# Kernel tuning notes

Hardware: AMD Instinct MI355X
Metric: run time of the kernel (lower is better)

The kernel has to match this reference:

```python
import jax, jax.numpy as jnp
import numpy as np

B, H, T, D = 2, 16, 2048, 64
BASE_WINDOW = 256
FULL = 999999


def _make_window_sizes(num_heads=H, base_window=BASE_WINDOW):
    ws = []
    for h in range(num_heads):
        if h < num_heads // 4:
            ws.append(base_window)
        elif h < num_heads // 2:
            ws.append(base_window * 2)
        elif h < 3 * num_heads // 4:
            ws.append(base_window * 4)
        else:
            ws.append(FULL)
    return jnp.asarray(ws, dtype=jnp.int32)


def setup_inputs() -> dict:
    key = jax.random.key(0)
    kq, kk, kv = jax.random.split(key, 3)
    Q = jax.random.normal(kq, (B, H, T, D), dtype=jnp.float32)
    K = jax.random.normal(kk, (B, H, T, D), dtype=jnp.float32)
    V = jax.random.normal(kv, (B, H, T, D), dtype=jnp.float32)
    return {"Q": Q, "K": K, "V": V, "window_sizes": _make_window_sizes()}


def reference(Q, K, V, window_sizes):
    b, h, t, d = Q.shape
    scale = 1.0 / np.sqrt(d).astype(np.float32)
    idx = jnp.arange(t, dtype=jnp.int32)
    diff = idx[:, None] - idx[None, :]  # [T, T], q_idx - kv_idx
    # causal & |q-k| <= w  ==  0 <= diff <= w  (per head)
    mask = (diff >= 0) & (diff[None, :, :] <= window_sizes[:, None, None])  # [H, T, T]
    scores = jnp.einsum('bhqd,bhkd->bhqk', Q, K) * scale  # [B, H, T, T]
    scores = jnp.where(mask[None], scores, -jnp.inf)
    attn = jax.nn.softmax(scores, axis=-1)
    return jnp.einsum('bhqk,bhkd->bhqd', attn, V)
```

## Files before the change

kernel.cpp:

```cpp
#include <hip/hip_runtime.h>
#include <hip/hip_bf16.h>


constexpr int Bc = 2, Hc = 16, Tc = 2048, Dc = 64;
constexpr int BQ = 64;
constexpr int BK = 32;
constexpr float QSCALE = 0.125f * 1.44269504088896340736f;
constexpr float CMAX = 16.0f;

constexpr size_t KB_OFF = 256;
constexpr size_t VB_OFF = 256 + (size_t)Bc * Hc * Tc * Dc * 2;
constexpr int HEADE = Tc * Dc;

constexpr int KOFF = 0;
constexpr int VOFF = 8192;

typedef __attribute__((ext_vector_type(8))) short short8;
typedef __attribute__((ext_vector_type(4))) float float4v;
typedef __attribute__((ext_vector_type(2))) unsigned int uint2v;

#if defined(__has_builtin)
#if __has_builtin(__builtin_amdgcn_exp2f)
#define EXP2 __builtin_amdgcn_exp2f
#endif
#endif
#ifndef EXP2
#define EXP2 exp2f
#endif

__device__ inline unsigned f2bf_u(float f) {
    union { float f; unsigned u; } v; v.f = f;
    return (v.u + 0x7fffu + ((v.u >> 16) & 1u)) >> 16;
}

__device__ inline short8 pack8(const float* t) {
    short8 r;
#pragma unroll
    for (int j = 0; j < 8; j++) r[j] = (short)f2bf_u(t[j]);
    return r;
}

__device__ inline unsigned pk_bf16(float a, float b) {
    __hip_bfloat162 h = __float22bfloat162_rn(make_float2(a, b));
    union { __hip_bfloat162 h; unsigned u; } v; v.h = h;
    return v.u;
}

__device__ inline short8 mk8(unsigned a0, unsigned a1, unsigned a2, unsigned a3) {
    union { unsigned u[4]; short8 s; } v;
    v.u[0] = a0; v.u[1] = a1; v.u[2] = a2; v.u[3] = a3;
    return v.s;
}

__global__ __launch_bounds__(256)
void preconv_kernel(const float* __restrict__ K, const float* __restrict__ V,
                    unsigned short* __restrict__ Kb, unsigned short* __restrict__ Vtb) {
    const int blk = blockIdx.x;
    const int tid = threadIdx.x;
    if (blk < 2048) {
        const int base = blk * 2048 + tid * 8;
        float4v a = *(const float4v*)(K + base);
        float4v b = *(const float4v*)(K + base + 4);
        float t[8] = {a[0], a[1], a[2], a[3], b[0], b[1], b[2], b[3]};
        *(short8*)(Kb + base) = pack8(t);
    } else {
        __shared__ float tile[64][65];
        const int blk2 = blk - 2048;
        const int bh = blk2 >> 5;
        const int t0 = (blk2 & 31) * 64;
        const float* src = V + (size_t)bh * HEADE + (size_t)t0 * Dc;
#pragma unroll
        for (int i = 0; i < 4; i++) {
            const int r = (tid >> 4) + i * 16;
            const int d4 = (tid & 15) * 4;
            float4v v4 = *(const float4v*)(src + r * Dc + d4);
            tile[r][d4] = v4[0]; tile[r][d4 + 1] = v4[1];
            tile[r][d4 + 2] = v4[2]; tile[r][d4 + 3] = v4[3];
        }
        __syncthreads();
        unsigned short* dst = Vtb + (size_t)bh * HEADE + t0;
#pragma unroll
        for (int i = 0; i < 2; i++) {
            const int d = (tid >> 3) + 32 * i;
            const int c = tid & 7;
            float t[8];
#pragma unroll
            for (int j = 0; j < 8; j++) t[j] = tile[c * 8 + j][d];
            *(short8*)(dst + (size_t)d * Tc + c * 8) = pack8(t);
        }
    }
}

__global__ __launch_bounds__(256, 4)
void dswa_kernel(const float* __restrict__ Q,
                 const unsigned short* __restrict__ Kb,
                 const unsigned short* __restrict__ Vtb,
                 const int* __restrict__ wsz,
                 float* __restrict__ O) {
    __shared__ __align__(16) unsigned short LDS[18432];

    const int tid  = threadIdx.x;
    const int wave = tid >> 6;
    const int g    = wave >> 1;
    const int wq   = wave & 1;
    const int lane = tid & 63;
    const int quad = lane >> 4;
    const int l16  = lane & 15;

    unsigned short* Kg = &LDS[KOFF + g * 4096];
    unsigned short* Vg = &LDS[VOFF + g * 5120];

    const int l128 = tid & 127;
    const int krow = l128 >> 2;
    const int kcol = (l128 & 3) * 16;
    const int vrow = l128 >> 1;
    const int vcol = (l128 & 1) * 16;

    const int blk  = blockIdx.x;
    const int ci   = blk & 255;
    const int slot = blk >> 8;
    const int b    = ci & 1;
    const int q5   = (ci >> 1) & 31;
    const int hh   = ci >> 6;
    const int h    = (3 - slot) * 4 + hh;
    const int qt   = (slot == 0) ? q5 : 31 - q5;
    const int q0   = qt * BQ;
    const int win  = wsz[h];

    const size_t headoff = (size_t)(b * Hc + h) * HEADE;
    const float* Qp = Q + headoff;
    const unsigned short* Kbh = Kb + headoff;
    const unsigned short* Vbh = Vtb + headoff;
    float* Op = O + headoff;

    short8 qf[2][2];
#pragma unroll
    for (int s = 0; s < 2; s++) {
        const int qrow = q0 + wq * 32 + s * 16 + l16;
#pragma unroll
        for (int c = 0; c < 2; c++) {
            const float* src = Qp + (size_t)qrow * Dc + c * 32 + quad * 8;
            float4v a = *(const float4v*)src;
            float4v d4 = *(const float4v*)(src + 4);
            float t[8] = {a[0]*QSCALE, a[1]*QSCALE, a[2]*QSCALE, a[3]*QSCALE,
                          d4[0]*QSCALE, d4[1]*QSCALE, d4[2]*QSCALE, d4[3]*QSCALE};
            qf[s][c] = pack8(t);
        }
    }

    float4v acc[2][4];
#pragma unroll
    for (int s = 0; s < 2; s++)
#pragma unroll
        for (int nb = 0; nb < 4; nb++) acc[s][nb] = (float4v){0.f, 0.f, 0.f, 0.f};
    float lp0 = 0.0f, lp1 = 0.0f;

    const int kv_lo = (max(0, q0 - win)) & ~(BK - 1);
    const int n_tiles = (q0 + BQ - kv_lo) >> 5;
    const int IT = (n_tiles + 1) >> 1;

    const int kv0g = kv_lo + g * BK;
    const unsigned short* kgp = Kbh + (size_t)(kv0g + krow) * Dc + kcol;
    const unsigned short* vgp = Vbh + (size_t)vrow * Tc + kv0g + vcol;

    short8 kr0, kr1, vr0, vr1;
    if (g < n_tiles) {
        kr0 = *(const short8*)(kgp);
        kr1 = *(const short8*)(kgp + 8);
        vr0 = *(const short8*)(vgp);
        vr1 = *(const short8*)(vgp + 8);
    }
    kgp += 64 * Dc; vgp += 64;

    for (int t = 0; t < IT; ++t) {
        const int ti = g + 2 * t;
        const bool act = ti < n_tiles;
        const int kv0 = kv_lo + ti * BK;
        unsigned short* Kl = Kg + (t & 1) * 2048;
        unsigned short* Vt = Vg + (t & 1) * 2560;

        if (act) {
            const int ks = (krow & 7) << 3;
            *(short8*)&Kl[krow * 64 + (kcol ^ ks)] = kr0;
            *(short8*)&Kl[krow * 64 + ((kcol + 8) ^ ks)] = kr1;
            *(short8*)&Vt[vrow * 40 + vcol] = vr0;
            *(short8*)&Vt[vrow * 40 + vcol + 8] = vr1;
        }
        __syncthreads();

        if (ti + 2 < n_tiles) {
            kr0 = *(const short8*)(kgp);
            kr1 = *(const short8*)(kgp + 8);
            vr0 = *(const short8*)(vgp);
            vr1 = *(const short8*)(vgp + 8);
        }
        kgp += 64 * Dc; vgp += 64;

        if (act) {
            float4v sT0[2], sT1[2];
#pragma unroll
            for (int mb = 0; mb < 2; mb++) {
                float4v c0 = {-CMAX, -CMAX, -CMAX, -CMAX};
                float4v c1 = {-CMAX, -CMAX, -CMAX, -CMAX};
#pragma unroll
                for (int ch = 0; ch < 2; ch++) {
                    const int row = mb * 16 + l16;
                    short8 kf = *(short8*)&Kl[row * 64 +
                                              ((ch * 32 + quad * 8) ^ ((row & 7) << 3))];
                    c0 = __builtin_amdgcn_mfma_f32_16x16x32_bf16(kf, qf[0][ch], c0, 0, 0, 0);
                    c1 = __builtin_amdgcn_mfma_f32_16x16x32_bf16(kf, qf[1][ch], c1, 0, 0, 0);
                }
                sT0[mb] = c0; sT1[mb] = c1;
            }

            short8 pf0, pf1;
            {
                const int rs = q0 + wq * 32;
                const bool interior = (kv0 + 31 <= rs) && (rs + 15 - kv0 <= win);
                if (!interior) {
                    const int dbase = rs + l16 - kv0 - quad * 4;
#pragma unroll
                    for (int mb = 0; mb < 2; mb++)
#pragma unroll
                        for (int r = 0; r < 4; r++) {
                            const unsigned diff = (unsigned)(dbase - mb * 16 - r);
                            sT0[mb][r] = (diff <= (unsigned)win) ? sT0[mb][r] : -3.0e38f;
                        }
                }
                unsigned w[4];
#pragma unroll
                for (int mb = 0; mb < 2; mb++) {
                    float p0 = EXP2(sT0[mb][0]);
                    float p1 = EXP2(sT0[mb][1]);
                    float p2 = EXP2(sT0[mb][2]);
                    float p3 = EXP2(sT0[mb][3]);
                    lp0 += (p0 + p1) + (p2 + p3);
                    w[2 * mb]     = pk_bf16(p0, p1);
                    w[2 * mb + 1] = pk_bf16(p2, p3);
                }
                uint2v pa = __builtin_amdgcn_permlane32_swap(w[0], w[2], false, false);
                uint2v c02 = __builtin_amdgcn_permlane16_swap(pa[0], pa[1], false, false);
                uint2v pb = __builtin_amdgcn_permlane32_swap(w[1], w[3], false, false);
                uint2v c13 = __builtin_amdgcn_permlane16_swap(pb[0], pb[1], false, false);
                pf0 = mk8(c02[0], c13[0], c02[1], c13[1]);
            }
            {
                const int rs = q0 + wq * 32 + 16;
                const bool interior = (kv0 + 31 <= rs) && (rs + 15 - kv0 <= win);
                if (!interior) {
                    const int dbase = rs + l16 - kv0 - quad * 4;
#pragma unroll
                    for (int mb = 0; mb < 2; mb++)
#pragma unroll
                        for (int r = 0; r < 4; r++) {
                            const unsigned diff = (unsigned)(dbase - mb * 16 - r);
                            sT1[mb][r] = (diff <= (unsigned)win) ? sT1[mb][r] : -3.0e38f;
                        }
                }
                unsigned w[4];
#pragma unroll
                for (int mb = 0; mb < 2; mb++) {
                    float p0 = EXP2(sT1[mb][0]);
                    float p1 = EXP2(sT1[mb][1]);
                    float p2 = EXP2(sT1[mb][2]);
                    float p3 = EXP2(sT1[mb][3]);
                    lp1 += (p0 + p1) + (p2 + p3);
                    w[2 * mb]     = pk_bf16(p0, p1);
                    w[2 * mb + 1] = pk_bf16(p2, p3);
                }
                uint2v pa = __builtin_amdgcn_permlane32_swap(w[0], w[2], false, false);
                uint2v c02 = __builtin_amdgcn_permlane16_swap(pa[0], pa[1], false, false);
                uint2v pb = __builtin_amdgcn_permlane32_swap(w[1], w[3], false, false);
                uint2v c13 = __builtin_amdgcn_permlane16_swap(pb[0], pb[1], false, false);
                pf1 = mk8(c02[0], c13[0], c02[1], c13[1]);
            }

#pragma unroll
            for (int nb = 0; nb < 4; nb++) {
                short8 vf = *(short8*)&Vt[(nb * 16 + l16) * 40 + quad * 8];
                acc[0][nb] = __builtin_amdgcn_mfma_f32_16x16x32_bf16(pf0, vf, acc[0][nb], 0, 0, 0);
                acc[1][nb] = __builtin_amdgcn_mfma_f32_16x16x32_bf16(pf1, vf, acc[1][nb], 0, 0, 0);
            }
        }
    }

    lp0 += __shfl_xor(lp0, 16); lp0 += __shfl_xor(lp0, 32);
    lp1 += __shfl_xor(lp1, 16); lp1 += __shfl_xor(lp1, 32);

    __syncthreads();
    float* fl = (float*)LDS;
    if (g == 1) {
#pragma unroll
        for (int s = 0; s < 2; s++) {
            if (quad == 0) fl[(wq * 32 + s * 16 + l16) * 66 + 64] = (s ? lp1 : lp0);
#pragma unroll
            for (int r = 0; r < 4; r++) {
                const int row = wq * 32 + s * 16 + quad * 4 + r;
#pragma unroll
                for (int nb = 0; nb < 4; nb++)
                    fl[row * 66 + nb * 16 + l16] = acc[s][nb][r];
            }
        }
    }
    __syncthreads();
    if (g == 0) {
#pragma unroll
        for (int s = 0; s < 2; s++) {
            const float lps = s ? lp1 : lp0;
#pragma unroll
            for (int r = 0; r < 4; r++) {
                const int row = wq * 32 + s * 16 + quad * 4 + r;
                const float l0 = __shfl(lps, quad * 4 + r);
                const float lt = l0 + fl[row * 66 + 64];
                const float inv = 1.0f / lt;
                float* dst = Op + (size_t)(q0 + row) * Dc;
#pragma unroll
                for (int nb = 0; nb < 4; nb++)
                    dst[nb * 16 + l16] = (acc[s][nb][r] + fl[row * 66 + nb * 16 + l16]) * inv;
            }
        }
    }
}

extern "C" void kernel_launch(void* const* d_in, const int* in_sizes, int n_in,
                              void* d_out, int out_size, void* d_ws, size_t ws_size,
                              hipStream_t stream) {
    (void)in_sizes; (void)n_in; (void)ws_size; (void)out_size;
    const float* Q = (const float*)d_in[0];
    const float* K = (const float*)d_in[1];
    const float* V = (const float*)d_in[2];
    const int* wsz = (const int*)d_in[3];
    float* Out = (float*)d_out;

    unsigned short* Kb  = (unsigned short*)((char*)d_ws + KB_OFF);
    unsigned short* Vtb = (unsigned short*)((char*)d_ws + VB_OFF);

    preconv_kernel<<<dim3(3072), dim3(256), 0, stream>>>(K, V, Kb, Vtb);
    dswa_kernel<<<dim3(1024), dim3(256), 0, stream>>>(Q, Kb, Vtb, wsz, Out);
}
```

Measured before the change: 120.7 us.

## Fuse K bf16 conversion into attention kernel and add MFMA priority hints

Result: no change. 119.3 us (-1.2%).

```diff
diff --git a/kernel.cpp b/kernel.cpp
--- a/kernel.cpp
+++ b/kernel.cpp
@@ -8,8 +8,7 @@
 constexpr float QSCALE = 0.125f * 1.44269504088896340736f;
 constexpr float CMAX = 16.0f;
 
-constexpr size_t KB_OFF = 256;
-constexpr size_t VB_OFF = 256 + (size_t)Bc * Hc * Tc * Dc * 2;
+constexpr size_t VB_OFF = 256;
 constexpr int HEADE = Tc * Dc;
 
 constexpr int KOFF = 0;
@@ -53,47 +52,37 @@
 }
 
 __global__ __launch_bounds__(256)
-void preconv_kernel(const float* __restrict__ K, const float* __restrict__ V,
-                    unsigned short* __restrict__ Kb, unsigned short* __restrict__ Vtb) {
-    const int blk = blockIdx.x;
+void preconv_kernel(const float* __restrict__ V, unsigned short* __restrict__ Vtb) {
+    __shared__ float tile[64][65];
+    const int blk2 = blockIdx.x;
     const int tid = threadIdx.x;
-    if (blk < 2048) {
-        const int base = blk * 2048 + tid * 8;
-        float4v a = *(const float4v*)(K + base);
-        float4v b = *(const float4v*)(K + base + 4);
-        float t[8] = {a[0], a[1], a[2], a[3], b[0], b[1], b[2], b[3]};
-        *(short8*)(Kb + base) = pack8(t);
-    } else {
-        __shared__ float tile[64][65];
-        const int blk2 = blk - 2048;
-        const int bh = blk2 >> 5;
-        const int t0 = (blk2 & 31) * 64;
-        const float* src = V + (size_t)bh * HEADE + (size_t)t0 * Dc;
-#pragma unroll
-        for (int i = 0; i < 4; i++) {
-            const int r = (tid >> 4) + i * 16;
-            const int d4 = (tid & 15) * 4;
-            float4v v4 = *(const float4v*)(src + r * Dc + d4);
-            tile[r][d4] = v4[0]; tile[r][d4 + 1] = v4[1];
-            tile[r][d4 + 2] = v4[2]; tile[r][d4 + 3] = v4[3];
-        }
-        __syncthreads();
-        unsigned short* dst = Vtb + (size_t)bh * HEADE + t0;
-#pragma unroll
-        for (int i = 0; i < 2; i++) {
-            const int d = (tid >> 3) + 32 * i;
-            const int c = tid & 7;
-            float t[8];
-#pragma unroll
-            for (int j = 0; j < 8; j++) t[j] = tile[c * 8 + j][d];
-            *(short8*)(dst + (size_t)d * Tc + c * 8) = pack8(t);
-        }
+    const int bh = blk2 >> 5;
+    const int t0 = (blk2 & 31) * 64;
+    const float* src = V + (size_t)bh * HEADE + (size_t)t0 * Dc;
+#pragma unroll
+    for (int i = 0; i < 4; i++) {
+        const int r = (tid >> 4) + i * 16;
+        const int d4 = (tid & 15) * 4;
+        float4v v4 = *(const float4v*)(src + r * Dc + d4);
+        tile[r][d4] = v4[0]; tile[r][d4 + 1] = v4[1];
+        tile[r][d4 + 2] = v4[2]; tile[r][d4 + 3] = v4[3];
+    }
+    __syncthreads();
+    unsigned short* dst = Vtb + (size_t)bh * HEADE + t0;
+#pragma unroll
+    for (int i = 0; i < 2; i++) {
+        const int d = (tid >> 3) + 32 * i;
+        const int c = tid & 7;
+        float t[8];
+#pragma unroll
+        for (int j = 0; j < 8; j++) t[j] = tile[c * 8 + j][d];
+        *(short8*)(dst + (size_t)d * Tc + c * 8) = pack8(t);
     }
 }
 
 __global__ __launch_bounds__(256, 4)
 void dswa_kernel(const float* __restrict__ Q,
-                 const unsigned short* __restrict__ Kb,
+                 const float* __restrict__ K,
                  const unsigned short* __restrict__ Vtb,
                  const int* __restrict__ wsz,
                  float* __restrict__ O) {
@@ -129,7 +118,7 @@
 
     const size_t headoff = (size_t)(b * Hc + h) * HEADE;
     const float* Qp = Q + headoff;
-    const unsigned short* Kbh = Kb + headoff;
+    const float* Kh = K + headoff;
     const unsigned short* Vbh = Vtb + headoff;
     float* Op = O + headoff;
 
@@ -160,13 +149,16 @@
     const int IT = (n_tiles + 1) >> 1;
 
     const int kv0g = kv_lo + g * BK;
-    const unsigned short* kgp = Kbh + (size_t)(kv0g + krow) * Dc + kcol;
+    const float* kgp = Kh + (size_t)(kv0g + krow) * Dc + kcol;
     const unsigned short* vgp = Vbh + (size_t)vrow * Tc + kv0g + vcol;
 
-    short8 kr0, kr1, vr0, vr1;
+    float4v ka0, ka1, ka2, ka3;
+    short8 vr0, vr1;
     if (g < n_tiles) {
-        kr0 = *(const short8*)(kgp);
-        kr1 = *(const short8*)(kgp + 8);
+        ka0 = *(const float4v*)(kgp);
+        ka1 = *(const float4v*)(kgp + 4);
+        ka2 = *(const float4v*)(kgp + 8);
+        ka3 = *(const float4v*)(kgp + 12);
         vr0 = *(const short8*)(vgp);
         vr1 = *(const short8*)(vgp + 8);
     }
@@ -181,6 +173,10 @@
 
         if (act) {
             const int ks = (krow & 7) << 3;
+            short8 kr0 = mk8(pk_bf16(ka0[0], ka0[1]), pk_bf16(ka0[2], ka0[3]),
+                             pk_bf16(ka1[0], ka1[1]), pk_bf16(ka1[2], ka1[3]));
+            short8 kr1 = mk8(pk_bf16(ka2[0], ka2[1]), pk_bf16(ka2[2], ka2[3]),
+                             pk_bf16(ka3[0], ka3[1]), pk_bf16(ka3[2], ka3[3]));
             *(short8*)&Kl[krow * 64 + (kcol ^ ks)] = kr0;
             *(short8*)&Kl[krow * 64 + ((kcol + 8) ^ ks)] = kr1;
             *(short8*)&Vt[vrow * 40 + vcol] = vr0;
@@ -189,8 +185,10 @@
         __syncthreads();
 
         if (ti + 2 < n_tiles) {
-            kr0 = *(const short8*)(kgp);
-            kr1 = *(const short8*)(kgp + 8);
+            ka0 = *(const float4v*)(kgp);
+            ka1 = *(const float4v*)(kgp + 4);
+            ka2 = *(const float4v*)(kgp + 8);
+            ka3 = *(const float4v*)(kgp + 12);
             vr0 = *(const short8*)(vgp);
             vr1 = *(const short8*)(vgp + 8);
         }
@@ -198,6 +196,7 @@
 
         if (act) {
             float4v sT0[2], sT1[2];
+            __builtin_amdgcn_s_setprio(1);
 #pragma unroll
             for (int mb = 0; mb < 2; mb++) {
                 float4v c0 = {-CMAX, -CMAX, -CMAX, -CMAX};
@@ -212,6 +211,7 @@
                 }
                 sT0[mb] = c0; sT1[mb] = c1;
             }
+            __builtin_amdgcn_s_setprio(0);
 
             short8 pf0, pf1;
             {
@@ -275,12 +275,14 @@
                 pf1 = mk8(c02[0], c13[0], c02[1], c13[1]);
             }
 
+            __builtin_amdgcn_s_setprio(1);
 #pragma unroll
             for (int nb = 0; nb < 4; nb++) {
                 short8 vf = *(short8*)&Vt[(nb * 16 + l16) * 40 + quad * 8];
                 acc[0][nb] = __builtin_amdgcn_mfma_f32_16x16x32_bf16(pf0, vf, acc[0][nb], 0, 0, 0);
                 acc[1][nb] = __builtin_amdgcn_mfma_f32_16x16x32_bf16(pf1, vf, acc[1][nb], 0, 0, 0);
             }
+            __builtin_amdgcn_s_setprio(0);
         }
     }
 
@@ -332,9 +334,8 @@
     const int* wsz = (const int*)d_in[3];
     float* Out = (float*)d_out;
 
-    unsigned short* Kb  = (unsigned short*)((char*)d_ws + KB_OFF);
     unsigned short* Vtb = (unsigned short*)((char*)d_ws + VB_OFF);
 
-    preconv_kernel<<<dim3(3072), dim3(256), 0, stream>>>(K, V, Kb, Vtb);
-    dswa_kernel<<<dim3(1024), dim3(256), 0, stream>>>(Q, Kb, Vtb, wsz, Out);
-}
+    preconv_kernel<<<dim3(1024), dim3(256), 0, stream>>>(V, Vtb);
+    dswa_kernel<<<dim3(1024), dim3(256), 0, stream>>>(Q, K, Vtb, wsz, Out);
+}
```

## Give each wave a private K/V LDS tile and drop per-tile block barriers

Applied to the files above, without the earlier changes.

Result: slower. 140.1 us (+16.1%).

```diff
diff --git a/kernel.cpp b/kernel.cpp
--- a/kernel.cpp
+++ b/kernel.cpp
@@ -11,9 +11,6 @@
 constexpr size_t KB_OFF = 256;
 constexpr size_t VB_OFF = 256 + (size_t)Bc * Hc * Tc * Dc * 2;
 constexpr int HEADE = Tc * Dc;
-
-constexpr int KOFF = 0;
-constexpr int VOFF = 8192;
 
 typedef __attribute__((ext_vector_type(8))) short short8;
 typedef __attribute__((ext_vector_type(4))) float float4v;
@@ -107,14 +104,12 @@
     const int quad = lane >> 4;
     const int l16  = lane & 15;
 
-    unsigned short* Kg = &LDS[KOFF + g * 4096];
-    unsigned short* Vg = &LDS[VOFF + g * 5120];
-
-    const int l128 = tid & 127;
-    const int krow = l128 >> 2;
-    const int kcol = (l128 & 3) * 16;
-    const int vrow = l128 >> 1;
-    const int vcol = (l128 & 1) * 16;
+    unsigned short* Kw = &LDS[wave * 4608];
+    unsigned short* Vw = &LDS[wave * 4608 + 2048];
+
+    const int krow  = lane >> 1;
+    const int kcolh = (lane & 1) * 32;
+    const int vrow  = lane;
 
     const int blk  = blockIdx.x;
     const int ci   = blk & 255;
@@ -156,132 +151,140 @@
     float lp0 = 0.0f, lp1 = 0.0f;
 
     const int kv_lo = (max(0, q0 - win)) & ~(BK - 1);
-    const int n_tiles = (q0 + BQ - kv_lo) >> 5;
-    const int IT = (n_tiles + 1) >> 1;
+    const int C = (q0 + BQ - kv_lo) >> 5;
 
     const int kv0g = kv_lo + g * BK;
-    const unsigned short* kgp = Kbh + (size_t)(kv0g + krow) * Dc + kcol;
-    const unsigned short* vgp = Vbh + (size_t)vrow * Tc + kv0g + vcol;
-
-    short8 kr0, kr1, vr0, vr1;
-    if (g < n_tiles) {
+    const unsigned short* kgp = Kbh + (size_t)(kv0g + krow) * Dc + kcolh;
+    const unsigned short* vgp = Vbh + (size_t)vrow * Tc + kv0g;
+
+    short8 kr0, kr1, kr2, kr3, vr0, vr1, vr2, vr3;
+    if (g < C) {
         kr0 = *(const short8*)(kgp);
         kr1 = *(const short8*)(kgp + 8);
+        kr2 = *(const short8*)(kgp + 16);
+        kr3 = *(const short8*)(kgp + 24);
         vr0 = *(const short8*)(vgp);
         vr1 = *(const short8*)(vgp + 8);
+        vr2 = *(const short8*)(vgp + 16);
+        vr3 = *(const short8*)(vgp + 24);
     }
     kgp += 64 * Dc; vgp += 64;
 
-    for (int t = 0; t < IT; ++t) {
-        const int ti = g + 2 * t;
-        const bool act = ti < n_tiles;
+    for (int ti = g; ti < C; ti += 2) {
         const int kv0 = kv_lo + ti * BK;
-        unsigned short* Kl = Kg + (t & 1) * 2048;
-        unsigned short* Vt = Vg + (t & 1) * 2560;
-
-        if (act) {
+
+        {
             const int ks = (krow & 7) << 3;
-            *(short8*)&Kl[krow * 64 + (kcol ^ ks)] = kr0;
-            *(short8*)&Kl[krow * 64 + ((kcol + 8) ^ ks)] = kr1;
-            *(short8*)&Vt[vrow * 40 + vcol] = vr0;
-            *(short8*)&Vt[vrow * 40 + vcol + 8] = vr1;
-        }
-        __syncthreads();
-
-        if (ti + 2 < n_tiles) {
+            *(short8*)&Kw[krow * 64 + ((kcolh)      ^ ks)] = kr0;
+            *(short8*)&Kw[krow * 64 + ((kcolh + 8)  ^ ks)] = kr1;
+            *(short8*)&Kw[krow * 64 + ((kcolh + 16) ^ ks)] = kr2;
+            *(short8*)&Kw[krow * 64 + ((kcolh + 24) ^ ks)] = kr3;
+            *(short8*)&Vw[vrow * 40 + 0]  = vr0;
+            *(short8*)&Vw[vrow * 40 + 8]  = vr1;
+            *(short8*)&Vw[vrow * 40 + 16] = vr2;
+            *(short8*)&Vw[vrow * 40 + 24] = vr3;
+        }
+
+        if (ti + 2 < C) {
             kr0 = *(const short8*)(kgp);
             kr1 = *(const short8*)(kgp + 8);
+            kr2 = *(const short8*)(kgp + 16);
+            kr3 = *(const short8*)(kgp + 24);
             vr0 = *(const short8*)(vgp);
             vr1 = *(const short8*)(vgp + 8);
+            vr2 = *(const short8*)(vgp + 16);
+            vr3 = *(const short8*)(vgp + 24);
         }
         kgp += 64 * Dc; vgp += 64;
 
-        if (act) {
-            float4v sT0[2], sT1[2];
+        float4v sT0[2], sT1[2];
+        __builtin_amdgcn_s_setprio(1);
+#pragma unroll
+        for (int mb = 0; mb < 2; mb++) {
+            float4v c0 = {-CMAX, -CMAX, -CMAX, -CMAX};
+            float4v c1 = {-CMAX, -CMAX, -CMAX, -CMAX};
+#pragma unroll
+            for (int ch = 0; ch < 2; ch++) {
+                const int row = mb * 16 + l16;
+                short8 kf = *(short8*)&Kw[row * 64 +
+                                          ((ch * 32 + quad * 8) ^ ((row & 7) << 3))];
+                c0 = __builtin_amdgcn_mfma_f32_16x16x32_bf16(kf, qf[0][ch], c0, 0, 0, 0);
+                c1 = __builtin_amdgcn_mfma_f32_16x16x32_bf16(kf, qf[1][ch], c1, 0, 0, 0);
+            }
+            sT0[mb] = c0; sT1[mb] = c1;
+        }
+        __builtin_amdgcn_s_setprio(0);
+
+        short8 pf0, pf1;
+        {
+            const int rs = q0 + wq * 32;
+            const bool interior = (kv0 + 31 <= rs) && (rs + 15 - kv0 <= win);
+            if (!interior) {
+                const int dbase = rs + l16 - kv0 - quad * 4;
+#pragma unroll
+                for (int mb = 0; mb < 2; mb++)
+#pragma unroll
+                    for (int r = 0; r < 4; r++) {
+                        const unsigned diff = (unsigned)(dbase - mb * 16 - r);
+                        sT0[mb][r] = (diff <= (unsigned)win) ? sT0[mb][r] : -3.0e38f;
+                    }
+            }
+            unsigned w[4];
 #pragma unroll
             for (int mb = 0; mb < 2; mb++) {
-                float4v c0 = {-CMAX, -CMAX, -CMAX, -CMAX};
-                float4v c1 = {-CMAX, -CMAX, -CMAX, -CMAX};
-#pragma unroll
-                for (int ch = 0; ch < 2; ch++) {
-                    const int row = mb * 16 + l16;
-                    short8 kf = *(short8*)&Kl[row * 64 +
-                                              ((ch * 32 + quad * 8) ^ ((row & 7) << 3))];
-                    c0 = __builtin_amdgcn_mfma_f32_16x16x32_bf16(kf, qf[0][ch], c0, 0, 0, 0);
-                    c1 = __builtin_amdgcn_mfma_f32_16x16x32_bf16(kf, qf[1][ch], c1, 0, 0, 0);
-                }
-                sT0[mb] = c0; sT1[mb] = c1;
-            }
-
-            short8 pf0, pf1;
-            {
-                const int rs = q0 + wq * 32;
-                const bool interior = (kv0 + 31 <= rs) && (rs + 15 - kv0 <= win);
-                if (!interior) {
-                    const int dbase = rs + l16 - kv0 - quad * 4;
-#pragma unroll
-                    for (int mb = 0; mb < 2; mb++)
-#pragma unroll
-                        for (int r = 0; r < 4; r++) {
-                            const unsigned diff = (unsigned)(dbase - mb * 16 - r);
-                            sT0[mb][r] = (diff <= (unsigned)win) ? sT0[mb][r] : -3.0e38f;
-                        }
-                }
-                unsigned w[4];
-#pragma unroll
-                for (int mb = 0; mb < 2; mb++) {
-                    float p0 = EXP2(sT0[mb][0]);
-                    float p1 = EXP2(sT0[mb][1]);
-                    float p2 = EXP2(sT0[mb][2]);
-                    float p3 = EXP2(sT0[mb][3]);
-                    lp0 += (p0 + p1) + (p2 + p3);
-                    w[2 * mb]     = pk_bf16(p0, p1);
-                    w[2 * mb + 1] = pk_bf16(p2, p3);
-                }
-                uint2v pa = __builtin_amdgcn_permlane32_swap(w[0], w[2], false, false);
-                uint2v c02 = __builtin_amdgcn_permlane16_swap(pa[0], pa[1], false, false);
-                uint2v pb = __builtin_amdgcn_permlane32_swap(w[1], w[3], false, false);
-                uint2v c13 = __builtin_amdgcn_permlane16_swap(pb[0], pb[1], false, false);
-                pf0 = mk8(c02[0], c13[0], c02[1], c13[1]);
-            }
-            {
-                const int rs = q0 + wq * 32 + 16;
-                const bool interior = (kv0 + 31 <= rs) && (rs + 15 - kv0 <= win);
-                if (!interior) {
-                    const int dbase = rs + l16 - kv0 - quad * 4;
-#pragma unroll
-                    for (int mb = 0; mb < 2; mb++)
-#pragma unroll
-                        for (int r = 0; r < 4; r++) {
-                            const unsigned diff = (unsigned)(dbase - mb * 16 - r);
-                            sT1[mb][r] = (diff <= (unsigned)win) ? sT1[mb][r] : -3.0e38f;
-                        }
-                }
-                unsigned w[4];
-#pragma unroll
-                for (int mb = 0; mb < 2; mb++) {
-                    float p0 = EXP2(sT1[mb][0]);
-                    float p1 = EXP2(sT1[mb][1]);
-                    float p2 = EXP2(sT1[mb][2]);
-                    float p3 = EXP2(sT1[mb][3]);
-                    lp1 += (p0 + p1) + (p2 + p3);
-                    w[2 * mb]     = pk_bf16(p0, p1);
-                    w[2 * mb + 1] = pk_bf16(p2, p3);
-                }
-                uint2v pa = __builtin_amdgcn_permlane32_swap(w[0], w[2], false, false);
-                uint2v c02 = __builtin_amdgcn_permlane16_swap(pa[0], pa[1], false, false);
-                uint2v pb = __builtin_amdgcn_permlane32_swap(w[1], w[3], false, false);
-                uint2v c13 = __builtin_amdgcn_permlane16_swap(pb[0], pb[1], false, false);
-                pf1 = mk8(c02[0], c13[0], c02[1], c13[1]);
-            }
-
-#pragma unroll
-            for (int nb = 0; nb < 4; nb++) {
-                short8 vf = *(short8*)&Vt[(nb * 16 + l16) * 40 + quad * 8];
-                acc[0][nb] = __builtin_amdgcn_mfma_f32_16x16x32_bf16(pf0, vf, acc[0][nb], 0, 0, 0);
-                acc[1][nb] = __builtin_amdgcn_mfma_f32_16x16x32_bf16(pf1, vf, acc[1][nb], 0, 0, 0);
-            }
-        }
+                float p0 = EXP2(sT0[mb][0]);
+                float p1 = EXP2(sT0[mb][1]);
+                float p2 = EXP2(sT0[mb][2]);
+                float p3 = EXP2(sT0[mb][3]);
+                lp0 += (p0 + p1) + (p2 + p3);
+                w[2 * mb]     = pk_bf16(p0, p1);
+                w[2 * mb + 1] = pk_bf16(p2, p3);
+            }
+            uint2v pa = __builtin_amdgcn_permlane32_swap(w[0], w[2], false, false);
+            uint2v c02 = __builtin_amdgcn_permlane16_swap(pa[0], pa[1], false, false);
+            uint2v pb = __builtin_amdgcn_permlane32_swap(w[1], w[3], false, false);
+            uint2v c13 = __builtin_amdgcn_permlane16_swap(pb[0], pb[1], false, false);
+            pf0 = mk8(c02[0], c13[0], c02[1], c13[1]);
+        }
+        {
+            const int rs = q0 + wq * 32 + 16;
+            const bool interior = (kv0 + 31 <= rs) && (rs + 15 - kv0 <= win);
+            if (!interior) {
+                const int dbase = rs + l16 - kv0 - quad * 4;
+#pragma unroll
+                for (int mb = 0; mb < 2; mb++)
+#pragma unroll
+                    for (int r = 0; r < 4; r++) {
+                        const unsigned diff = (unsigned)(dbase - mb * 16 - r);
+                        sT1[mb][r] = (diff <= (unsigned)win) ? sT1[mb][r] : -3.0e38f;
+                    }
+            }
+            unsigned w[4];
+#pragma unroll
+            for (int mb = 0; mb < 2; mb++) {
+                float p0 = EXP2(sT1[mb][0]);
+                float p1 = EXP2(sT1[mb][1]);
+                float p2 = EXP2(sT1[mb][2]);
+                float p3 = EXP2(sT1[mb][3]);
+                lp1 += (p0 + p1) + (p2 + p3);
+                w[2 * mb]     = pk_bf16(p0, p1);
+                w[2 * mb + 1] = pk_bf16(p2, p3);
+            }
+            uint2v pa = __builtin_amdgcn_permlane32_swap(w[0], w[2], false, false);
+            uint2v c02 = __builtin_amdgcn_permlane16_swap(pa[0], pa[1], false, false);
+            uint2v pb = __builtin_amdgcn_permlane32_swap(w[1], w[3], false, false);
+            uint2v c13 = __builtin_amdgcn_permlane16_swap(pb[0], pb[1], false, false);
+            pf1 = mk8(c02[0], c13[0], c02[1], c13[1]);
+        }
+
+        __builtin_amdgcn_s_setprio(1);
+#pragma unroll
+        for (int nb = 0; nb < 4; nb++) {
+            short8 vf = *(short8*)&Vw[(nb * 16 + l16) * 40 + quad * 8];
+            acc[0][nb] = __builtin_amdgcn_mfma_f32_16x16x32_bf16(pf0, vf, acc[0][nb], 0, 0, 0);
+            acc[1][nb] = __builtin_amdgcn_mfma_f32_16x16x32_bf16(pf1, vf, acc[1][nb], 0, 0, 0);
+        }
+        __builtin_amdgcn_s_setprio(0);
     }
 
     lp0 += __shfl_xor(lp0, 16); lp0 += __shfl_xor(lp0, 32);
```

## Split KV tiles across four wave groups with 512-thread blocks

Applied to the files above, without the earlier changes.

Measured after the change: 258.8 us. 114% more time.

```diff
diff --git a/kernel.cpp b/kernel.cpp
--- a/kernel.cpp
+++ b/kernel.cpp
@@ -11,9 +11,6 @@
 constexpr size_t KB_OFF = 256;
 constexpr size_t VB_OFF = 256 + (size_t)Bc * Hc * Tc * Dc * 2;
 constexpr int HEADE = Tc * Dc;
-
-constexpr int KOFF = 0;
-constexpr int VOFF = 8192;
 
 typedef __attribute__((ext_vector_type(8))) short short8;
 typedef __attribute__((ext_vector_type(4))) float float4v;
@@ -91,7 +88,7 @@
     }
 }
 
-__global__ __launch_bounds__(256, 4)
+__global__ __launch_bounds__(512, 8)
 void dswa_kernel(const float* __restrict__ Q,
                  const unsigned short* __restrict__ Kb,
                  const unsigned short* __restrict__ Vtb,
@@ -107,8 +104,8 @@
     const int quad = lane >> 4;
     const int l16  = lane & 15;
 
-    unsigned short* Kg = &LDS[KOFF + g * 4096];
-    unsigned short* Vg = &LDS[VOFF + g * 5120];
+    unsigned short* Kg = &LDS[g * 2048];
+    unsigned short* Vg = &LDS[8192 + g * 2560];
 
     const int l128 = tid & 127;
     const int krow = l128 >> 2;
@@ -156,48 +153,47 @@
     float lp0 = 0.0f, lp1 = 0.0f;
 
     const int kv_lo = (max(0, q0 - win)) & ~(BK - 1);
-    const int n_tiles = (q0 + BQ - kv_lo) >> 5;
-    const int IT = (n_tiles + 1) >> 1;
+    const int C = (q0 + BQ - kv_lo) >> 5;
+    const int IT = (C + 3) >> 2;
 
     const int kv0g = kv_lo + g * BK;
     const unsigned short* kgp = Kbh + (size_t)(kv0g + krow) * Dc + kcol;
     const unsigned short* vgp = Vbh + (size_t)vrow * Tc + kv0g + vcol;
 
     short8 kr0, kr1, vr0, vr1;
-    if (g < n_tiles) {
+    if (g < C) {
         kr0 = *(const short8*)(kgp);
         kr1 = *(const short8*)(kgp + 8);
         vr0 = *(const short8*)(vgp);
         vr1 = *(const short8*)(vgp + 8);
     }
-    kgp += 64 * Dc; vgp += 64;
+    kgp += 128 * Dc; vgp += 128;
 
     for (int t = 0; t < IT; ++t) {
-        const int ti = g + 2 * t;
-        const bool act = ti < n_tiles;
+        const int ti = g + 4 * t;
+        const bool act = ti < C;
         const int kv0 = kv_lo + ti * BK;
-        unsigned short* Kl = Kg + (t & 1) * 2048;
-        unsigned short* Vt = Vg + (t & 1) * 2560;
 
         if (act) {
             const int ks = (krow & 7) << 3;
-            *(short8*)&Kl[krow * 64 + (kcol ^ ks)] = kr0;
-            *(short8*)&Kl[krow * 64 + ((kcol + 8) ^ ks)] = kr1;
-            *(short8*)&Vt[vrow * 40 + vcol] = vr0;
-            *(short8*)&Vt[vrow * 40 + vcol + 8] = vr1;
+            *(short8*)&Kg[krow * 64 + (kcol ^ ks)] = kr0;
+            *(short8*)&Kg[krow * 64 + ((kcol + 8) ^ ks)] = kr1;
+            *(short8*)&Vg[vrow * 40 + vcol] = vr0;
+            *(short8*)&Vg[vrow * 40 + vcol + 8] = vr1;
         }
         __syncthreads();
 
-        if (ti + 2 < n_tiles) {
+        if (ti + 4 < C) {
             kr0 = *(const short8*)(kgp);
             kr1 = *(const short8*)(kgp + 8);
             vr0 = *(const short8*)(vgp);
             vr1 = *(const short8*)(vgp + 8);
         }
-        kgp += 64 * Dc; vgp += 64;
+        kgp += 128 * Dc; vgp += 128;
 
         if (act) {
             float4v sT0[2], sT1[2];
+            __builtin_amdgcn_s_setprio(1);
 #pragma unroll
             for (int mb = 0; mb < 2; mb++) {
                 float4v c0 = {-CMAX, -CMAX, -CMAX, -CMAX};
@@ -205,13 +201,14 @@
 #pragma unroll
                 for (int ch = 0; ch < 2; ch++) {
                     const int row = mb * 16 + l16;
-                    short8 kf = *(short8*)&Kl[row * 64 +
+                    short8 kf = *(short8*)&Kg[row * 64 +
                                               ((ch * 32 + quad * 8) ^ ((row & 7) << 3))];
                     c0 = __builtin_amdgcn_mfma_f32_16x16x32_bf16(kf, qf[0][ch], c0, 0, 0, 0);
                     c1 = __builtin_amdgcn_mfma_f32_16x16x32_bf16(kf, qf[1][ch], c1, 0, 0, 0);
                 }
                 sT0[mb] = c0; sT1[mb] = c1;
             }
+            __builtin_amdgcn_s_setprio(0);
 
             short8 pf0, pf1;
             {
@@ -275,30 +272,78 @@
                 pf1 = mk8(c02[0], c13[0], c02[1], c13[1]);
             }
 
+            __builtin_amdgcn_s_setprio(1);
 #pragma unroll
             for (int nb = 0; nb < 4; nb++) {
-                short8 vf = *(short8*)&Vt[(nb * 16 + l16) * 40 + quad * 8];
+                short8 vf = *(short8*)&Vg[(nb * 16 + l16) * 40 + quad * 8];
                 acc[0][nb] = __builtin_amdgcn_mfma_f32_16x16x32_bf16(pf0, vf, acc[0][nb], 0, 0, 0);
                 acc[1][nb] = __builtin_amdgcn_mfma_f32_16x16x32_bf16(pf1, vf, acc[1][nb], 0, 0, 0);
             }
-        }
+            __builtin_amdgcn_s_setprio(0);
+        }
+        __syncthreads();
     }
 
     lp0 += __shfl_xor(lp0, 16); lp0 += __shfl_xor(lp0, 32);
     lp1 += __shfl_xor(lp1, 16); lp1 += __shfl_xor(lp1, 32);
 
+    float* fA = (float*)LDS;
+    float* fB = fA + 4224;
+    if (g == 1 || g == 3) {
+        float* fx = (g == 1) ? fA : fB;
+#pragma unroll
+        for (int s = 0; s < 2; s++) {
+            if (quad == 0) fx[(wq * 32 + s * 16 + l16) * 66 + 64] = (s ? lp1 : lp0);
+#pragma unroll
+            for (int r = 0; r < 4; r++) {
+                const int row = wq * 32 + s * 16 + quad * 4 + r;
+#pragma unroll
+                for (int nb = 0; nb < 4; nb++)
+                    fx[row * 66 + nb * 16 + l16] = acc[s][nb][r];
+            }
+        }
+    }
     __syncthreads();
-    float* fl = (float*)LDS;
-    if (g == 1) {
+    float lt0[2][4];
+    if (g == 0) {
 #pragma unroll
         for (int s = 0; s < 2; s++) {
-            if (quad == 0) fl[(wq * 32 + s * 16 + l16) * 66 + 64] = (s ? lp1 : lp0);
-#pragma unroll
-            for (int r = 0; r < 4; r++) {
-                const int row = wq * 32 + s * 16 + quad * 4 + r;
-#pragma unroll
-                for (int nb = 0; nb < 4; nb++)
-                    fl[row * 66 + nb * 16 + l16] = acc[s][nb][r];
+            const float lps = s ? lp1 : lp0;
+#pragma unroll
+            for (int r = 0; r < 4; r++) {
+                const int row = wq * 32 + s * 16 + quad * 4 + r;
+                lt0[s][r] = __shfl(lps, quad * 4 + r) + fA[row * 66 + 64];
+#pragma unroll
+                for (int nb = 0; nb < 4; nb++)
+                    acc[s][nb][r] += fA[row * 66 + nb * 16 + l16];
+            }
+        }
+    }
+    if (g == 2) {
+#pragma unroll
+        for (int s = 0; s < 2; s++)
+#pragma unroll
+            for (int r = 0; r < 4; r++) {
+                const int row = wq * 32 + s * 16 + quad * 4 + r;
+#pragma unroll
+                for (int nb = 0; nb < 4; nb++)
+                    acc[s][nb][r] += fB[row * 66 + nb * 16 + l16];
+            }
+    }
+    __syncthreads();
+    if (g == 2) {
+#pragma unroll
+        for (int s = 0; s < 2; s++) {
+            if (quad == 0) {
+                const int row = wq * 32 + s * 16 + l16;
+                fA[row * 66 + 64] = (s ? lp1 : lp0) + fB[row * 66 + 64];
+            }
+#pragma unroll
+            for (int r = 0; r < 4; r++) {
+                const int row = wq * 32 + s * 16 + quad * 4 + r;
+#pragma unroll
+                for (int nb = 0; nb < 4; nb++)
+                    fA[row * 66 + nb * 16 + l16] = acc[s][nb][r];
             }
         }
     }
@@ -306,17 +351,15 @@
     if (g == 0) {
 #pragma unroll
         for (int s = 0; s < 2; s++) {
-            const float lps = s ? lp1 : lp0;
-#pragma unroll
-            for (int r = 0; r < 4; r++) {
-                const int row = wq * 32 + s * 16 + quad * 4 + r;
-                const float l0 = __shfl(lps, quad * 4 + r);
-                const float lt = l0 + fl[row * 66 + 64];
+#pragma unroll
+            for (int r = 0; r < 4; r++) {
+                const int row = wq * 32 + s * 16 + quad * 4 + r;
+                const float lt = lt0[s][r] + fA[row * 66 + 64];
                 const float inv = 1.0f / lt;
                 float* dst = Op + (size_t)(q0 + row) * Dc;
 #pragma unroll
                 for (int nb = 0; nb < 4; nb++)
-                    dst[nb * 16 + l16] = (acc[s][nb][r] + fl[row * 66 + nb * 16 + l16]) * inv;
+                    dst[nb * 16 + l16] = (acc[s][nb][r] + fA[row * 66 + nb * 16 + l16]) * inv;
             }
         }
     }
@@ -336,5 +379,5 @@
     unsigned short* Vtb = (unsigned short*)((char*)d_ws + VB_OFF);
 
     preconv_kernel<<<dim3(3072), dim3(256), 0, stream>>>(K, V, Kb, Vtb);
-    dswa_kernel<<<dim3(1024), dim3(256), 0, stream>>>(Q, Kb, Vtb, wsz, Out);
-}
+    dswa_kernel<<<dim3(1024), dim3(512), 0, stream>>>(Q, Kb, Vtb, wsz, Out);
+}
```
